# Kernel optimization log

Measured on AMD Instinct MI355X. Metric: run time of the kernel, lower is better.

Reference implementation:

```python
import jax, jax.numpy as jnp
import numpy as np
import math

B, T, D = 2, 2048, 2048
NH, HD = 16, 128          # n_heads, head_dim (expand_factor=1)
LAMBDA_INIT = 0.8 - 0.6 * math.exp(-0.3 * 0)  # layer_depth=0 -> 0.2
EPS = float(jnp.finfo(jnp.float32).eps)


def rms_norm(x):
    return x * jax.lax.rsqrt(jnp.mean(x * x, axis=-1, keepdims=True) + EPS)


def apply_rotary(x, cos, sin):
    # x: (B,T,H,HD); cos/sin: (1,T,1,HD/2); half-split convention
    d = x.shape[-1] // 2
    x1, x2 = x[..., :d], x[..., d:]
    return jnp.concatenate([x1 * cos + x2 * sin, -x1 * sin + x2 * cos], axis=-1)


def causal_attn(q, k, v, scale):
    # q,k: (B,T,H,HD); v: (B,T,H,Dv) -> (B,T,H,Dv)
    Tq = q.shape[1]
    s = jnp.einsum('bqhd,bkhd->bhqk', q, k) * scale
    mask = jnp.tril(jnp.ones((Tq, Tq), dtype=bool))
    s = jnp.where(mask, s, -1e30)
    p = jax.nn.softmax(s, axis=-1)
    return jnp.einsum('bhqk,bkhd->bqhd', p, v)


def setup_inputs():
    key = jax.random.key(0)
    ks = jax.random.split(key, 8)
    x = jax.random.normal(ks[0], (B, T, D), jnp.float32)
    Wq = jax.random.normal(ks[1], (D, NH * HD), jnp.float32) * 0.02
    Wk = jax.random.normal(ks[2], (D, NH * HD), jnp.float32) * 0.02
    Wv = jax.random.normal(ks[3], (D, NH * HD), jnp.float32) * 0.02
    lambda_q1 = jax.random.normal(ks[4], (HD // 2,), jnp.float32) * 0.1
    lambda_k1 = jax.random.normal(ks[5], (HD // 2,), jnp.float32) * 0.1
    lambda_q2 = jax.random.normal(ks[6], (HD // 2,), jnp.float32) * 0.1
    lambda_k2 = jax.random.normal(ks[7], (HD // 2,), jnp.float32) * 0.1
    softmax_scaler = jnp.ones((1, 1, NH, 1), jnp.float32)
    return {"x": x, "Wq": Wq, "Wk": Wk, "Wv": Wv,
            "lambda_q1": lambda_q1, "lambda_k1": lambda_k1,
            "lambda_q2": lambda_q2, "lambda_k2": lambda_k2,
            "softmax_scaler": softmax_scaler}


def reference(x, Wq, Wk, Wv, lambda_q1, lambda_k1, lambda_q2, lambda_k2, softmax_scaler):
    b, t, _ = x.shape
    q = (x @ Wq).reshape(b, t, NH, HD)
    k = (x @ Wk).reshape(b, t, NH, HD)
    v = (x @ Wv).reshape(b, t, NH // 2, 2 * HD)

    # rotary tables (base 10000, dim=HD)
    inv_freq = 1.0 / (10000.0 ** (jnp.arange(0, HD, 2, dtype=jnp.float32) / HD))
    freqs = jnp.arange(t, dtype=jnp.float32)[:, None] * inv_freq[None, :]
    cos = jnp.cos(freqs)[None, :, None, :]
    sin = jnp.sin(freqs)[None, :, None, :]

    # qk-norm then RoPE
    q = apply_rotary(rms_norm(q), cos, sin)
    k = apply_rotary(rms_norm(k), cos, sin)

    k = k.reshape(b, t, 2, NH // 2, HD)
    k1, k2 = k[:, :, 0], k[:, :, 1]

    # scalable softmax: scale q by s * log(position)
    log_pos = jnp.log(jnp.arange(1, t + 1, dtype=jnp.float32)).reshape(1, t, 1, 1)
    q = softmax_scaler * log_pos * q

    q = q.reshape(b, t, 2, NH // 2, HD)
    q1, q2 = q[:, :, 0], q[:, :, 1]

    scale = 1.0 / math.sqrt(HD)  # flash-attn default: 1/sqrt(q head dim)
    y1 = causal_attn(q1, k1, v, scale)
    y2 = causal_attn(q2, k2, v, scale)

    lambda_1 = jnp.exp(jnp.sum(lambda_q1 * lambda_k1))
    lambda_2 = jnp.exp(jnp.sum(lambda_q2 * lambda_k2))
    lambda_full = lambda_1 - lambda_2 + LAMBDA_INIT

    y = (y1 - lambda_full * y2).reshape(b, t, D)
    return y
```

## Files before the change

### kernel.cpp

```cpp
#include <hip/hip_runtime.h>

typedef unsigned short u16;
typedef _Float16 f16;
typedef __attribute__((ext_vector_type(8))) _Float16 half8;
typedef __attribute__((ext_vector_type(4))) _Float16 half4;
typedef __attribute__((ext_vector_type(4))) float f32x4;

#define B_  2
#define T_  2048
#define D_  2048
#define NH_ 16
#define HD_ 128
#define QBLK 64
#define KBLK 32

#define MFMAH(a,b,c) __builtin_amdgcn_mfma_f32_16x16x32_f16((a),(b),(c),0,0,0)

__device__ __forceinline__ void gll16(void* lds, const void* g) {
  __builtin_amdgcn_global_load_lds(
      (const __attribute__((address_space(1))) unsigned int*)(size_t)(g),
      (__attribute__((address_space(3))) unsigned int*)(unsigned int)(size_t)(lds),
      16, 0, 0);
}

__global__ __launch_bounds__(256)
void cast_x_kernel(const float* __restrict__ X, f16* __restrict__ Xb) {
  size_t i = ((size_t)blockIdx.x * 256 + threadIdx.x) * 8;
  float4 v0 = *(const float4*)(X + i);
  float4 v1 = *(const float4*)(X + i + 4);
  half8 o;
  o[0] = (f16)v0.x; o[1] = (f16)v0.y; o[2] = (f16)v0.z; o[3] = (f16)v0.w;
  o[4] = (f16)v1.x; o[5] = (f16)v1.y; o[6] = (f16)v1.z; o[7] = (f16)v1.w;
  *(half8*)(Xb + i) = o;
}

__global__ __launch_bounds__(256)
void wt_kernel(const float* __restrict__ Wq, const float* __restrict__ Wk,
               const float* __restrict__ Wv, f16* __restrict__ Wt) {
  __shared__ float tile[32][33];
  const int z = blockIdx.z;
  const float* W = z == 0 ? Wq : (z == 1 ? Wk : Wv);
  f16* O = Wt + (size_t)z * (2048 * 2048);
  int k0 = blockIdx.x * 32, n0 = blockIdx.y * 32;
  int tx = threadIdx.x & 31, ty = threadIdx.x >> 5;
#pragma unroll
  for (int s = 0; s < 4; ++s)
    tile[ty + s * 8][tx] = W[(size_t)(k0 + ty + s * 8) * 2048 + n0 + tx];
  __syncthreads();
#pragma unroll
  for (int s = 0; s < 4; ++s) {
    int nrow = n0 + ty + s * 8;
    int orow = nrow;
    if (z < 2) {
      int hh = nrow >> 7, dd = nrow & 127;
      orow = (hh << 7) | ((dd & 63) << 1) | (dd >> 6);
    }
    O[(size_t)orow * 2048 + k0 + tx] = (f16)tile[tx][ty + s * 8];
  }
}

__global__ void rope_table_kernel(float* __restrict__ cosT, float* __restrict__ sinT,
                                  float* __restrict__ logT) {
  int t = blockIdx.x, d = threadIdx.x;
  float invf = exp2f(-(float)d * (13.287712379549449f / 64.f));
  float fr = (float)t * invf;
  cosT[t * 64 + d] = cosf(fr);
  sinT[t * 64 + d] = sinf(fr);
  if (d == 0) logT[t] = logf((float)(t + 1));
}

__global__ void lambda_kernel(const float* __restrict__ lq1, const float* __restrict__ lk1,
                              const float* __restrict__ lq2, const float* __restrict__ lk2,
                              float* __restrict__ lam) {
  int l = threadIdx.x;
  float a = lq1[l] * lk1[l];
  float b = lq2[l] * lk2[l];
#pragma unroll
  for (int off = 1; off < 64; off <<= 1) { a += __shfl_xor(a, off); b += __shfl_xor(b, off); }
  if (l == 0) lam[0] = expf(a) - expf(b) + 0.2f;
}

__global__ __launch_bounds__(256)
void gemm_qkv_kernel(const f16* __restrict__ Xb, const f16* __restrict__ Wt,
                     const float* __restrict__ cosT, const float* __restrict__ sinT,
                     const float* __restrict__ logT,
                     const float* __restrict__ scaler,
                     f16* __restrict__ Qp, f16* __restrict__ Kp,
                     f16* __restrict__ Vt) {
  __shared__ f16 As[2][128 * 32];
  __shared__ f16 Bs[2][128 * 32];
  __shared__ float ps[4][64];
  const int bid = blockIdx.x, z = blockIdx.y;
  const int lid = ((bid & 7) << 6) | (bid >> 3);
  const int bn = lid >> 5, bm = lid & 31;
  const f16* Bw = Wt + (size_t)z * (2048 * 2048);
  const int tid = threadIdx.x;
  const int w = tid >> 6, l = tid & 63;
  const int li = l & 15, lg = l >> 4;
  const int wr = w >> 1, wc = w & 1;

  f32x4 acc[4][4] = {};

  const int o0 = (w * 2 + 0) * 1024 + l * 16;
  const int o1 = (w * 2 + 1) * 1024 + l * 16;
  const int rA0 = o0 >> 6, rA1 = o1 >> 6;
  const int cs0 = ((o0 >> 4) & 3) ^ (rA0 & 3);
  const int cs1 = ((o1 >> 4) & 3) ^ (rA1 & 3);
  const f16* srcA0 = Xb + (size_t)(bm * 128 + rA0) * 2048 + cs0 * 8;
  const f16* srcA1 = Xb + (size_t)(bm * 128 + rA1) * 2048 + cs1 * 8;
  const f16* srcB0 = Bw + (size_t)(bn * 128 + rA0) * 2048 + cs0 * 8;
  const f16* srcB1 = Bw + (size_t)(bn * 128 + rA1) * 2048 + cs1 * 8;
  const int c0 = (w * 2 + 0) * 1024, c1 = (w * 2 + 1) * 1024;

#define GSTAGE(bi, kt)                                         \
  do {                                                         \
    gll16((char*)As[bi] + c0, srcA0 + (kt) * 32);              \
    gll16((char*)As[bi] + c1, srcA1 + (kt) * 32);              \
    gll16((char*)Bs[bi] + c0, srcB0 + (kt) * 32);              \
    gll16((char*)Bs[bi] + c1, srcB1 + (kt) * 32);              \
  } while (0)

  GSTAGE(0, 0);
  for (int kt = 0; kt < 64; ++kt) {
    const int cur = kt & 1;
    if (kt < 63) {
      GSTAGE(cur ^ 1, kt + 1);
      asm volatile("s_waitcnt vmcnt(4)" ::: "memory");
    } else {
      asm volatile("s_waitcnt vmcnt(0)" ::: "memory");
    }
    __builtin_amdgcn_s_barrier();
    half8 af[4], bfr[4];
#pragma unroll
    for (int mi = 0; mi < 4; ++mi) {
      int row = wr * 64 + mi * 16 + li;
      int ch = lg ^ (row & 3);
      af[mi] = *(const half8*)((const char*)As[cur] + row * 64 + ch * 16);
    }
#pragma unroll
    for (int ni = 0; ni < 4; ++ni) {
      int row = wc * 64 + ni * 16 + li;
      int ch = lg ^ (row & 3);
      bfr[ni] = *(const half8*)((const char*)Bs[cur] + row * 64 + ch * 16);
    }
    __builtin_amdgcn_s_setprio(1);
#pragma unroll
    for (int mi = 0; mi < 4; ++mi)
#pragma unroll
      for (int ni = 0; ni < 4; ++ni)
        acc[mi][ni] = MFMAH(af[mi], bfr[ni], acc[mi][ni]);
    __builtin_amdgcn_s_setprio(0);
    __builtin_amdgcn_s_barrier();
  }
#undef GSTAGE

  if (z == 2) {
#pragma unroll
    for (int mi = 0; mi < 4; ++mi) {
      const int m0 = bm * 128 + wr * 64 + mi * 16 + lg * 4;
      const int b = m0 >> 11, t0 = m0 & 2047;
#pragma unroll
      for (int ni = 0; ni < 4; ++ni) {
        const int n = bn * 128 + wc * 64 + ni * 16 + li;
        const int hv = n >> 8, dv = n & 255;
        half4 pk;
        pk[0] = (f16)acc[mi][ni][0]; pk[1] = (f16)acc[mi][ni][1];
        pk[2] = (f16)acc[mi][ni][2]; pk[3] = (f16)acc[mi][ni][3];
        *(half4*)(Vt + ((size_t)(b * 8 + hv) * 256 + dv) * 2048 + t0) = pk;
      }
    }
    return;
  }

  float ss[4][4];
#pragma unroll
  for (int mi = 0; mi < 4; ++mi)
#pragma unroll
    for (int r = 0; r < 4; ++r) {
      float s = acc[mi][0][r] * acc[mi][0][r] + acc[mi][1][r] * acc[mi][1][r] +
                acc[mi][2][r] * acc[mi][2][r] + acc[mi][3][r] * acc[mi][3][r];
      s += __shfl_xor(s, 1);
      s += __shfl_xor(s, 2);
      s += __shfl_xor(s, 4);
      s += __shfl_xor(s, 8);
      ss[mi][r] = s;
    }
  if (li == 0) {
#pragma unroll
    for (int mi = 0; mi < 4; ++mi)
#pragma unroll
      for (int r = 0; r < 4; ++r)
        ps[w][mi * 16 + lg * 4 + r] = ss[mi][r];
  }
  __syncthreads();

  const int h = bn;
  f16* dst = z ? Kp : Qp;
  const float sch = scaler[h] * 0.08838834764831845f;
#pragma unroll
  for (int mi = 0; mi < 4; ++mi) {
#pragma unroll
    for (int r = 0; r < 4; ++r) {
      const int m = bm * 128 + wr * 64 + mi * 16 + lg * 4 + r;
      const int t = m & 2047, b = m >> 11;
      const int idx = mi * 16 + lg * 4 + r;
      const float tot = ps[wr * 2][idx] + ps[wr * 2 + 1][idx];
      const float rr = rsqrtf(tot * (1.f / 128.f) + 1.1920929e-07f);
      const float lm = z ? 1.f : sch * logT[t];
      f16* drow = dst + ((size_t)(b * 16 + h) * 2048 + t) * 128;
#pragma unroll
      for (int ni = 0; ni < 4; ++ni) {
        const int n = wc * 64 + ni * 16 + li;
        const int d1 = n >> 1;
        const float c = cosT[t * 64 + d1], s = sinT[t * 64 + d1];
        float v = acc[mi][ni][r] * rr;
        float vp = __shfl_xor(v, 1);
        float o = (li & 1) ? (v * c - vp * s) : (v * c + vp * s);
        o *= lm;
        drow[d1 + (li & 1) * 64] = (f16)o;
      }
    }
  }
}

__global__ __launch_bounds__(256, 2)
void attn_kernel(const f16* __restrict__ Qp, const f16* __restrict__ Kp,
                 const f16* __restrict__ Vt,
                 f16* __restrict__ Y1, f16* __restrict__ Y2) {
  __shared__ f16 Ks[2][KBLK * 128];
  __shared__ f16 Vs[2][256 * KBLK];
  __shared__ f16 Ps[4][16 * 32];

  const int bid = blockIdx.x;
  const int lid = ((bid & 7) << 6) | (bid >> 3);
  const int pr = lid & 15;
  const int bh = lid >> 4;
  const int b = bh >> 4, h = bh & 15;
  const int grp = h >> 3, hv = h & 7;
  const f16* QhP = Qp + (size_t)bh * (T_ * HD_);
  const f16* KhP = Kp + (size_t)bh * (T_ * HD_);
  const f16* Vh = Vt + (size_t)(b * 8 + hv) * (256 * T_);
  f16* Ybase = (grp ? Y2 : Y1) + (size_t)(b * 8 + hv) * T_ * 256;

  const int tid = threadIdx.x;
  const int w = tid >> 6, l = tid & 63;
  const int li = l & 15, lg = l >> 4;

  int kRow[2], kCs[2], vDv[4], vCs[4];
#pragma unroll
  for (int i = 0; i < 2; ++i) {
    int o = (w * 2 + i) * 1024 + l * 16;
    kRow[i] = o >> 8;
    kCs[i] = ((o >> 4) & 15) ^ (kRow[i] & 7);
  }
#pragma unroll
  for (int i = 0; i < 4; ++i) {
    int o = (w * 4 + i) * 1024 + l * 16;
    vDv[i] = o >> 6;
    vCs[i] = ((o >> 4) & 3) ^ ((vDv[i] >> 1) & 3);
  }

#define STAGE(bi, kv0)                                                          \
  do {                                                                          \
    _Pragma("unroll")                                                           \
    for (int i = 0; i < 2; ++i)                                                 \
      gll16((char*)Ks[bi] + (w * 2 + i) * 1024,                                 \
            KhP + (size_t)((kv0) + kRow[i]) * 128 + kCs[i] * 8);                \
    _Pragma("unroll")                                                           \
    for (int i = 0; i < 4; ++i)                                                 \
      gll16((char*)Vs[bi] + (w * 4 + i) * 1024,                                 \
            Vh + (size_t)vDv[i] * T_ + (kv0) + vCs[i] * 8);                     \
  } while (0)

  const float L2E = 1.4426950408889634f;

#pragma unroll 1
  for (int t2 = 0; t2 < 2; ++t2) {
    const int qt = t2 ? pr : 31 - pr;
    const int q0 = qt * QBLK + w * 16;

    STAGE(0, 0);

    half8 qf[4];
    {
      const f16* qrow = QhP + (size_t)(q0 + li) * 128;
#pragma unroll
      for (int kc = 0; kc < 4; ++kc)
        qf[kc] = *(const half8*)(qrow + kc * 32 + lg * 8);
    }
    f32x4 acc[16] = {};
    float m[4], se[4];
#pragma unroll
    for (int r = 0; r < 4; ++r) { m[r] = -1e30f; se[r] = 0.f; }

    const int nkv = (qt + 1) * 2;
    for (int kv = 0; kv < nkv; ++kv) {
      const int kv0 = kv * KBLK;
      const int cur = kv & 1;
      if (kv + 1 < nkv) {
        STAGE(cur ^ 1, kv0 + KBLK);
        asm volatile("s_waitcnt vmcnt(6)" ::: "memory");
      } else {
        asm volatile("s_waitcnt vmcnt(0)" ::: "memory");
      }
      __builtin_amdgcn_s_barrier();
      if (kv0 <= q0 + 15) {
        f32x4 s0 = {}, s1 = {}, s0b = {}, s1b = {};
        __builtin_amdgcn_s_setprio(1);
#pragma unroll
        for (int kc = 0; kc < 2; ++kc) {
          int ch = kc * 4 + lg;
          int off0 = li * 256 + ((ch ^ (li & 7)) * 16);
          int off1 = (li + 16) * 256 + ((ch ^ (li & 7)) * 16);
          const half8 k0 = *(const half8*)((const char*)Ks[cur] + off0);
          const half8 k1 = *(const half8*)((const char*)Ks[cur] + off1);
          s0 = MFMAH(qf[kc], k0, s0);
          s1 = MFMAH(qf[kc], k1, s1);
        }
#pragma unroll
        for (int kc = 2; kc < 4; ++kc) {
          int ch = kc * 4 + lg;
          int off0 = li * 256 + ((ch ^ (li & 7)) * 16);
          int off1 = (li + 16) * 256 + ((ch ^ (li & 7)) * 16);
          const half8 k0 = *(const half8*)((const char*)Ks[cur] + off0);
          const half8 k1 = *(const half8*)((const char*)Ks[cur] + off1);
          s0b = MFMAH(qf[kc], k0, s0b);
          s1b = MFMAH(qf[kc], k1, s1b);
        }
        __builtin_amdgcn_s_setprio(0);
        s0 += s0b; s1 += s1b;

        float v0[4], v1[4], tmx[4];
        const bool nomask = (kv0 + 31 <= q0);
#pragma unroll
        for (int r = 0; r < 4; ++r) {
          float a = s0[r], bb = s1[r];
          if (!nomask) {
            const int qr = q0 + lg * 4 + r;
            if (kv0 + li > qr) a = -1e30f;
            if (kv0 + 16 + li > qr) bb = -1e30f;
          }
          float t = fmaxf(a, bb);
          t = fmaxf(t, __shfl_xor(t, 1));
          t = fmaxf(t, __shfl_xor(t, 2));
          t = fmaxf(t, __shfl_xor(t, 4));
          t = fmaxf(t, __shfl_xor(t, 8));
          v0[r] = a; v1[r] = bb; tmx[r] = t;
        }
        int need = (tmx[0] > m[0] + 8.f) | (tmx[1] > m[1] + 8.f) |
                   (tmx[2] > m[2] + 8.f) | (tmx[3] > m[3] + 8.f);
        if (__any(need)) {
          float corr[4];
#pragma unroll
          for (int r = 0; r < 4; ++r) {
            float mn = fmaxf(m[r], tmx[r]);
            corr[r] = exp2f((m[r] - mn) * L2E);
            m[r] = mn;
            se[r] *= corr[r];
          }
#pragma unroll
          for (int nt = 0; nt < 16; ++nt) {
            f32x4 a = acc[nt];
            a[0] *= corr[0]; a[1] *= corr[1]; a[2] *= corr[2]; a[3] *= corr[3];
            acc[nt] = a;
          }
        }
        f16* Pw = &Ps[w][0];
#pragma unroll
        for (int r = 0; r < 4; ++r) {
          float p0 = exp2f((v0[r] - m[r]) * L2E);
          float p1 = exp2f((v1[r] - m[r]) * L2E);
          float rs = p0 + p1;
          rs += __shfl_xor(rs, 1);
          rs += __shfl_xor(rs, 2);
          rs += __shfl_xor(rs, 4);
          rs += __shfl_xor(rs, 8);
          se[r] += rs;
          const int rowA = lg * 4 + r;
          const int x = (rowA >> 1) & 3;
          Pw[rowA * 32 + (((li >> 3) ^ x) * 8) + (li & 7)] = (f16)p0;
          Pw[rowA * 32 + ((((li >> 3) | 2) ^ x) * 8) + (li & 7)] = (f16)p1;
        }
        const half8 pa = *(const half8*)(Pw + li * 32 + ((lg ^ ((li >> 1) & 3)) * 8));
        __builtin_amdgcn_s_setprio(1);
#pragma unroll
        for (int nt = 0; nt < 16; ++nt) {
          const int dv = nt * 16 + li;
          const int ch = lg ^ ((dv >> 1) & 3);
          const half8 vf = *(const half8*)((const char*)Vs[cur] + dv * 64 + ch * 16);
          acc[nt] = MFMAH(pa, vf, acc[nt]);
        }
        __builtin_amdgcn_s_setprio(0);
      }
      __builtin_amdgcn_s_barrier();
    }
    float inv[4];
#pragma unroll
    for (int r = 0; r < 4; ++r) inv[r] = 1.0f / se[r];
    f16* Yout = Ybase + (size_t)(qt * QBLK) * 256;
#pragma unroll
    for (int nt = 0; nt < 16; ++nt)
#pragma unroll
      for (int r = 0; r < 4; ++r)
        Yout[(size_t)(w * 16 + lg * 4 + r) * 256 + nt * 16 + li] =
            (f16)(acc[nt][r] * inv[r]);
  }
#undef STAGE
}

__global__ __launch_bounds__(256)
void combine_kernel(const f16* __restrict__ Y1, const f16* __restrict__ Y2,
                    const float* __restrict__ lamp, float* __restrict__ out) {
  size_t f = ((size_t)blockIdx.x * 256 + threadIdx.x) * 8;
  int dv = (int)(f & 255);
  int hv = (int)((f >> 8) & 7);
  size_t bt = f >> 11;
  int t = (int)(bt & 2047);
  int b = (int)(bt >> 11);
  const float lam = lamp[0];
  size_t yi = ((size_t)(b * 8 + hv) * 2048 + t) * 256 + dv;
  half8 a = *(const half8*)(Y1 + yi);
  half8 c = *(const half8*)(Y2 + yi);
  float4 o0, o1;
  o0.x = (float)a[0] - lam * (float)c[0];
  o0.y = (float)a[1] - lam * (float)c[1];
  o0.z = (float)a[2] - lam * (float)c[2];
  o0.w = (float)a[3] - lam * (float)c[3];
  o1.x = (float)a[4] - lam * (float)c[4];
  o1.y = (float)a[5] - lam * (float)c[5];
  o1.z = (float)a[6] - lam * (float)c[6];
  o1.w = (float)a[7] - lam * (float)c[7];
  *(float4*)(out + f) = o0;
  *(float4*)(out + f + 4) = o1;
}

extern "C" void kernel_launch(void* const* d_in, const int* in_sizes, int n_in,
                              void* d_out, int out_size, void* d_ws, size_t ws_size,
                              hipStream_t stream) {
  const float* x   = (const float*)d_in[0];
  const float* Wq  = (const float*)d_in[1];
  const float* Wk  = (const float*)d_in[2];
  const float* Wv  = (const float*)d_in[3];
  const float* lq1 = (const float*)d_in[4];
  const float* lk1 = (const float*)d_in[5];
  const float* lq2 = (const float*)d_in[6];
  const float* lk2 = (const float*)d_in[7];
  const float* scl = (const float*)d_in[8];
  float* out = (float*)d_out;

  char* ws = (char*)d_ws;
  f16*  Xb  = (f16*)(ws + 0);
  f16*  Wt  = (f16*)(ws + 16777216);
  f16*  Qp  = (f16*)(ws + 41943040);
  f16*  Kp  = (f16*)(ws + 58720256);
  f16*  Vt  = (f16*)(ws + 75497472);
  f16*  Y1  = (f16*)(ws + 92274688);
  f16*  Y2  = (f16*)(ws + 109051904);
  float* cosT = (float*)(ws + 125829120);
  float* sinT = (float*)(ws + 126353408);
  float* logT = (float*)(ws + 126877696);
  float* lam  = (float*)(ws + 126885888);

  cast_x_kernel<<<4096, 256, 0, stream>>>(x, Xb);
  wt_kernel<<<dim3(64, 64, 3), 256, 0, stream>>>(Wq, Wk, Wv, Wt);
  rope_table_kernel<<<2048, 64, 0, stream>>>(cosT, sinT, logT);
  lambda_kernel<<<1, 64, 0, stream>>>(lq1, lk1, lq2, lk2, lam);
  gemm_qkv_kernel<<<dim3(512, 3), 256, 0, stream>>>(Xb, Wt, cosT, sinT, logT, scl, Qp, Kp, Vt);
  attn_kernel<<<512, 256, 0, stream>>>(Qp, Kp, Vt, Y1, Y2);
  combine_kernel<<<4096, 256, 0, stream>>>(Y1, Y2, lam, out);
}
```

Measured before the change: 343.6 us.

## Load GEMM B operand directly from global into registers, bypassing LDS

The QKV projection GEMM no longer stages the weight tile through shared memory. Each wave loads its B fragments straight from global memory into registers, double-buffered across two k-steps, while the A tile still goes through LDS. This halves LDS usage and LDS traffic, and the launch bounds now request 3 blocks per CU. The trade-off is uncoalesced-ish direct global loads for B (each row read by 2 waves), more register pressure, and stalls on register loads that arrive without any LDS-level sharing.

```diff
diff --git a/kernel.cpp b/kernel.cpp
--- a/kernel.cpp
+++ b/kernel.cpp
@@ -80,7 +80,7 @@
   if (l == 0) lam[0] = expf(a) - expf(b) + 0.2f;
 }
 
-__global__ __launch_bounds__(256)
+__global__ __launch_bounds__(256, 3)
 void gemm_qkv_kernel(const f16* __restrict__ Xb, const f16* __restrict__ Wt,
                      const float* __restrict__ cosT, const float* __restrict__ sinT,
                      const float* __restrict__ logT,
@@ -88,7 +88,6 @@
                      f16* __restrict__ Qp, f16* __restrict__ Kp,
                      f16* __restrict__ Vt) {
   __shared__ f16 As[2][128 * 32];
-  __shared__ f16 Bs[2][128 * 32];
   __shared__ float ps[4][64];
   const int bid = blockIdx.x, z = blockIdx.y;
   const int lid = ((bid & 7) << 6) | (bid >> 3);
@@ -108,51 +107,73 @@
   const int cs1 = ((o1 >> 4) & 3) ^ (rA1 & 3);
   const f16* srcA0 = Xb + (size_t)(bm * 128 + rA0) * 2048 + cs0 * 8;
   const f16* srcA1 = Xb + (size_t)(bm * 128 + rA1) * 2048 + cs1 * 8;
-  const f16* srcB0 = Bw + (size_t)(bn * 128 + rA0) * 2048 + cs0 * 8;
-  const f16* srcB1 = Bw + (size_t)(bn * 128 + rA1) * 2048 + cs1 * 8;
   const int c0 = (w * 2 + 0) * 1024, c1 = (w * 2 + 1) * 1024;
 
-#define GSTAGE(bi, kt)                                         \
-  do {                                                         \
-    gll16((char*)As[bi] + c0, srcA0 + (kt) * 32);              \
-    gll16((char*)As[bi] + c1, srcA1 + (kt) * 32);              \
-    gll16((char*)Bs[bi] + c0, srcB0 + (kt) * 32);              \
-    gll16((char*)Bs[bi] + c1, srcB1 + (kt) * 32);              \
+  const f16* bp0 = Bw + (size_t)(bn * 128 + wc * 64 + 0 * 16 + li) * 2048 + lg * 8;
+  const f16* bp1 = Bw + (size_t)(bn * 128 + wc * 64 + 1 * 16 + li) * 2048 + lg * 8;
+  const f16* bp2 = Bw + (size_t)(bn * 128 + wc * 64 + 2 * 16 + li) * 2048 + lg * 8;
+  const f16* bp3 = Bw + (size_t)(bn * 128 + wc * 64 + 3 * 16 + li) * 2048 + lg * 8;
+
+#define ASTAGE(bi, kt)                                  \
+  do {                                                  \
+    gll16((char*)As[bi] + c0, srcA0 + (kt) * 32);       \
+    gll16((char*)As[bi] + c1, srcA1 + (kt) * 32);       \
   } while (0)
-
-  GSTAGE(0, 0);
-  for (int kt = 0; kt < 64; ++kt) {
-    const int cur = kt & 1;
-    if (kt < 63) {
-      GSTAGE(cur ^ 1, kt + 1);
-      asm volatile("s_waitcnt vmcnt(4)" ::: "memory");
+#define BLOAD(dst, kt)                                  \
+  do {                                                  \
+    dst[0] = *(const half8*)(bp0 + (kt) * 32);          \
+    dst[1] = *(const half8*)(bp1 + (kt) * 32);          \
+    dst[2] = *(const half8*)(bp2 + (kt) * 32);          \
+    dst[3] = *(const half8*)(bp3 + (kt) * 32);          \
+  } while (0)
+#define AREAD(bi)                                                           \
+  do {                                                                      \
+    _Pragma("unroll")                                                       \
+    for (int mi = 0; mi < 4; ++mi) {                                        \
+      int row = wr * 64 + mi * 16 + li;                                     \
+      int ch = lg ^ (row & 3);                                              \
+      af[mi] = *(const half8*)((const char*)As[bi] + row * 64 + ch * 16);   \
+    }                                                                       \
+  } while (0)
+#define MM(bfr)                                                    \
+  do {                                                             \
+    __builtin_amdgcn_s_setprio(1);                                 \
+    _Pragma("unroll")                                              \
+    for (int mi = 0; mi < 4; ++mi)                                 \
+      _Pragma("unroll")                                            \
+      for (int ni = 0; ni < 4; ++ni)                               \
+        acc[mi][ni] = MFMAH(af[mi], bfr[ni], acc[mi][ni]);         \
+    __builtin_amdgcn_s_setprio(0);                                 \
+  } while (0)
+
+  half8 af[4], bfrA[4], bfrB[4];
+  ASTAGE(0, 0);
+  BLOAD(bfrA, 0);
+  for (int j = 0; j < 32; ++j) {
+    const int kt1 = 2 * j + 1;
+    ASTAGE(1, kt1);
+    asm volatile("s_waitcnt vmcnt(2)" ::: "memory");
+    __builtin_amdgcn_s_barrier();
+    AREAD(0);
+    BLOAD(bfrB, kt1);
+    MM(bfrA);
+    __builtin_amdgcn_s_barrier();
+    if (j < 31) {
+      ASTAGE(0, kt1 + 1);
+      asm volatile("s_waitcnt vmcnt(2)" ::: "memory");
     } else {
       asm volatile("s_waitcnt vmcnt(0)" ::: "memory");
     }
     __builtin_amdgcn_s_barrier();
-    half8 af[4], bfr[4];
-#pragma unroll
-    for (int mi = 0; mi < 4; ++mi) {
-      int row = wr * 64 + mi * 16 + li;
-      int ch = lg ^ (row & 3);
-      af[mi] = *(const half8*)((const char*)As[cur] + row * 64 + ch * 16);
-    }
-#pragma unroll
-    for (int ni = 0; ni < 4; ++ni) {
-      int row = wc * 64 + ni * 16 + li;
-      int ch = lg ^ (row & 3);
-      bfr[ni] = *(const half8*)((const char*)Bs[cur] + row * 64 + ch * 16);
-    }
-    __builtin_amdgcn_s_setprio(1);
-#pragma unroll
-    for (int mi = 0; mi < 4; ++mi)
-#pragma unroll
-      for (int ni = 0; ni < 4; ++ni)
-        acc[mi][ni] = MFMAH(af[mi], bfr[ni], acc[mi][ni]);
-    __builtin_amdgcn_s_setprio(0);
+    AREAD(1);
+    if (j < 31) BLOAD(bfrA, kt1 + 1);
+    MM(bfrB);
     __builtin_amdgcn_s_barrier();
   }
-#undef GSTAGE
+#undef ASTAGE
+#undef BLOAD
+#undef AREAD
+#undef MM
 
   if (z == 2) {
 #pragma unroll
```

New measurement: 424.7 us. 1.24x slower.
